# Performance work log

Hardware: AMD Instinct MI355X
Metric: run time of the kernel (lower is better)

Reference implementation:

```python
import jax, jax.numpy as jnp
import numpy as np

NUM_HEADS = 16
WINDOW = 256


def setup_inputs() -> dict:
    key = jax.random.key(0)
    ks = jax.random.split(key, 4)
    B, S, D = 1, 4096, 1024
    scale = 1.0 / np.sqrt(D)  # keep logits sane with random weights
    x = jax.random.normal(ks[0], (B, S, D), dtype=jnp.float32)
    Wq = jax.random.normal(ks[1], (D, D), dtype=jnp.float32) * scale
    Wk = jax.random.normal(ks[2], (D, D), dtype=jnp.float32) * scale
    Wv = jax.random.normal(ks[3], (D, D), dtype=jnp.float32) * scale
    bq = jnp.zeros((D,), dtype=jnp.float32)
    bk = jnp.zeros((D,), dtype=jnp.float32)
    bv = jnp.zeros((D,), dtype=jnp.float32)
    return {"x": x, "Wq": Wq, "bq": bq, "Wk": Wk, "bk": bk, "Wv": Wv, "bv": bv}


def reference(x, Wq, bq, Wk, bk, Wv, bv):
    B, S, D = x.shape
    H = NUM_HEADS
    depth = D // H

    def split_heads(t):
        return t.reshape(B, S, H, depth).transpose(0, 2, 1, 3)  # [B,H,S,depth]

    # torch nn.Linear: y = x @ W.T + b
    Q = split_heads(x @ Wq.T + bq)
    K = split_heads(x @ Wk.T + bk)
    V = split_heads(x @ Wv.T + bv)

    scores = jnp.einsum("bhqd,bhkd->bhqk", Q, K) / jnp.sqrt(jnp.float32(depth))
    idx = jnp.arange(S)
    band = jnp.abs(idx[None, :] - idx[:, None]) <= WINDOW  # [S,S] local window
    scores = jnp.where(band[None, None], scores, -jnp.inf)
    attn = jax.nn.softmax(scores, axis=-1)
    out = jnp.einsum("bhqk,bhkd->bhqd", attn, V)
    return out.transpose(0, 2, 1, 3).reshape(B, S, D)
```

## Files before the change

### kernel.cpp

```cpp
#include <hip/hip_runtime.h>
#include <hip/hip_bf16.h>

typedef __attribute__((ext_vector_type(4))) float f32x4;
typedef __attribute__((ext_vector_type(16))) float f32x16;
typedef __attribute__((ext_vector_type(8))) short s16x8;
typedef __attribute__((ext_vector_type(4))) float float4_t;
typedef __attribute__((ext_vector_type(2))) unsigned int u32x2;

union U8 { s16x8 v; unsigned u[4]; };

__device__ __forceinline__ ushort f2bf(float f) {
  union { float f; unsigned u; } v; v.f = f;
  unsigned r = v.u + 0x7fffu + ((v.u >> 16) & 1u);
  return (ushort)(r >> 16);
}

__device__ __forceinline__ void async_copy16(ushort* lds, const ushort* g) {
  __builtin_amdgcn_global_load_lds(
      (const __attribute__((address_space(1))) unsigned int*)g,
      (__attribute__((address_space(3))) unsigned int*)lds, 16, 0, 0);
}

__device__ __forceinline__ unsigned lds_addr(const void* p) {
  return (unsigned)(unsigned long long)(__attribute__((address_space(3))) const void*)p;
}

#define TRRD(dst, addr, off_lit) \
  asm volatile("ds_read_b64_tr_b16 %0, %1 offset:" #off_lit : "=v"(dst) : "v"(addr))

__global__ __launch_bounds__(256) void convert_kernel(
    const float* __restrict__ x, const float* __restrict__ Wq,
    const float* __restrict__ Wk, const float* __restrict__ Wv,
    ushort* __restrict__ xs, ushort* __restrict__ ws) {
  int b = blockIdx.x;
  if (b < 2048) {
    int c = b * 256 + threadIdx.x;
    int kc = c & 127;
    int m = c >> 7;
    const float4_t* s = (const float4_t*)&x[(size_t)m * 1024 + kc * 8];
    float4_t a0 = s[0], a1 = s[1];
    s16x8 v;
    v[0] = (short)f2bf(a0[0]); v[1] = (short)f2bf(a0[1]);
    v[2] = (short)f2bf(a0[2]); v[3] = (short)f2bf(a0[3]);
    v[4] = (short)f2bf(a1[0]); v[5] = (short)f2bf(a1[1]);
    v[6] = (short)f2bf(a1[2]); v[7] = (short)f2bf(a1[3]);
    int tm = m >> 7, tk = kc >> 3, r = m & 127, c8 = kc & 7;
    *(s16x8*)&xs[((size_t)(tm * 16 + tk) * 128 + r) * 64 + ((c8 ^ (r & 7)) * 8)] = v;
  } else {
    int c = (b - 2048) * 256 + threadIdx.x;
    int kc = c & 127;
    int n = c >> 7;
    int p = n >> 10, nW = n & 1023;
    const float* __restrict__ W = (p == 0) ? Wq : (p == 1) ? Wk : Wv;
    const float4_t* s = (const float4_t*)&W[(size_t)nW * 1024 + kc * 8];
    float4_t a0 = s[0], a1 = s[1];
    s16x8 v;
    v[0] = (short)f2bf(a0[0]); v[1] = (short)f2bf(a0[1]);
    v[2] = (short)f2bf(a0[2]); v[3] = (short)f2bf(a0[3]);
    v[4] = (short)f2bf(a1[0]); v[5] = (short)f2bf(a1[1]);
    v[6] = (short)f2bf(a1[2]); v[7] = (short)f2bf(a1[3]);
    unsigned tn3 = (unsigned)n / 192u;
    unsigned r = (unsigned)n - tn3 * 192u;
    int tk = kc >> 3, c8 = kc & 7;
    *(s16x8*)&ws[((size_t)(tn3 * 16 + tk) * 192 + r) * 64 + ((c8 ^ (r & 7)) * 8)] = v;
  }
}

__global__ __launch_bounds__(256, 2) void qkv_gemm_kernel(
    const ushort* __restrict__ xs, const ushort* __restrict__ wsb,
    const float* __restrict__ bq, const float* __restrict__ bk,
    const float* __restrict__ bv, ushort* __restrict__ qkv) {
  __shared__ ushort lA[2][8192];
  __shared__ ushort lB[2][12288];
  const int t = threadIdx.x;
  const int lane = t & 63, w = t >> 6;
  const int wm = w >> 1, wn = w & 1;
  const int l15 = lane & 15, l4 = lane >> 4;
  const int phys = blockIdx.x;
  const int swz = (phys & 7) * 64 + (phys >> 3);
  const int xcd = swz >> 6, jj = swz & 63;
  const int bm = (xcd >> 1) * 8 + (jj >> 3);
  const int bn = (xcd & 1) * 8 + (jj & 7);

  const ushort* Apan = xs + (size_t)bm * 16 * 8192;
  const ushort* Bpan = wsb + (size_t)bn * 16 * 12288;

  f32x4 acc[4][6];
#pragma unroll
  for (int i = 0; i < 4; i++)
#pragma unroll
    for (int j = 0; j < 6; j++) acc[i][j] = (f32x4)0.f;

#define STAGE_A(buf, kt)                                                        \
  do {                                                                          \
    const ushort* s0 = Apan + (size_t)(kt) * 8192;                              \
    _Pragma("unroll") for (int i_ = 0; i_ < 4; i_++)                            \
      async_copy16(&lA[buf][(t + i_ * 256) * 8], s0 + (t + i_ * 256) * 8);      \
  } while (0)
#define STAGE_B(buf, kt)                                                        \
  do {                                                                          \
    const ushort* s2 = Bpan + (size_t)(kt) * 12288;                             \
    _Pragma("unroll") for (int i_ = 0; i_ < 6; i_++)                            \
      async_copy16(&lB[buf][(t + i_ * 256) * 8], s2 + (t + i_ * 256) * 8);      \
  } while (0)

  STAGE_A(0, 0);
  STAGE_B(0, 0);
  asm volatile("s_waitcnt vmcnt(0)");
  __builtin_amdgcn_s_barrier();

  for (int kt = 0; kt < 16; ++kt) {
    const int cur = kt & 1;
    s16x8 af[4], bfr[6];
#pragma unroll
    for (int mi = 0; mi < 4; mi++) {
      int ra = wm * 64 + mi * 16 + l15;
      int g = l4 ^ (ra & 7);
      af[mi] = *(const s16x8*)&lA[cur][ra * 64 + g * 8];
    }
#pragma unroll
    for (int ni = 0; ni < 6; ni++) {
      int rb = wn * 96 + ni * 16 + l15;
      int g = l4 ^ (rb & 7);
      bfr[ni] = *(const s16x8*)&lB[cur][rb * 64 + g * 8];
    }
    if (kt + 1 < 16) STAGE_A(cur ^ 1, kt + 1);
    asm volatile("s_waitcnt lgkmcnt(0)");
    __builtin_amdgcn_sched_barrier(0);
    __builtin_amdgcn_s_setprio(1);
#pragma unroll
    for (int mi = 0; mi < 4; mi++)
#pragma unroll
      for (int ni = 0; ni < 6; ni++)
        acc[mi][ni] = __builtin_amdgcn_mfma_f32_16x16x32_bf16(af[mi], bfr[ni], acc[mi][ni], 0, 0, 0);
    __builtin_amdgcn_s_setprio(0);
#pragma unroll
    for (int mi = 0; mi < 4; mi++) {
      int ra = wm * 64 + mi * 16 + l15;
      int g = (4 + l4) ^ (ra & 7);
      af[mi] = *(const s16x8*)&lA[cur][ra * 64 + g * 8];
    }
#pragma unroll
    for (int ni = 0; ni < 6; ni++) {
      int rb = wn * 96 + ni * 16 + l15;
      int g = (4 + l4) ^ (rb & 7);
      bfr[ni] = *(const s16x8*)&lB[cur][rb * 64 + g * 8];
    }
    if (kt + 1 < 16) STAGE_B(cur ^ 1, kt + 1);
    asm volatile("s_waitcnt lgkmcnt(0)");
    __builtin_amdgcn_sched_barrier(0);
    __builtin_amdgcn_s_setprio(1);
#pragma unroll
    for (int mi = 0; mi < 4; mi++)
#pragma unroll
      for (int ni = 0; ni < 6; ni++)
        acc[mi][ni] = __builtin_amdgcn_mfma_f32_16x16x32_bf16(af[mi], bfr[ni], acc[mi][ni], 0, 0, 0);
    __builtin_amdgcn_s_setprio(0);
    asm volatile("s_waitcnt vmcnt(0)");
    __builtin_amdgcn_s_barrier();
  }
#undef STAGE_A
#undef STAGE_B

#pragma unroll
  for (int ni = 0; ni < 6; ni++) {
    int col = bn * 192 + wn * 96 + ni * 16 + l15;
    int p = col >> 10;
    const float* bias = (p == 0) ? bq : (p == 1) ? bk : bv;
    float b = bias[col & 1023];
    float qscale = (p == 0) ? 0.125f * 1.44269504f : 1.0f;
    int h = (col >> 6) & 15, dd = col & 63;
    size_t base = ((size_t)(p * 16 + h) * 4096) * 64 + dd;
#pragma unroll
    for (int mi = 0; mi < 4; mi++) {
#pragma unroll
      for (int r = 0; r < 4; r++) {
        int s = bm * 128 + wm * 64 + mi * 16 + l4 * 4 + r;
        float v = (acc[mi][ni][r] + b) * qscale;
        qkv[base + (size_t)s * 64] = f2bf(v);
      }
    }
  }
}

__global__ __launch_bounds__(256) void attn_local_kernel(
    const ushort* __restrict__ qkv, float* __restrict__ out) {
  __shared__ ushort lds[2][2][4096];
  const int bid = blockIdx.x;
  const int wid = (bid & 7) * 64 + (bid >> 3);
  const int hd = wid >> 5;
  const int q0 = (wid & 31) << 7;
  const int t = threadIdx.x;
  const int lane = t & 63, w = t >> 6;
  const int l15 = lane & 15, l31 = lane & 31;
  const int b4 = (lane >> 4) & 1, hf = lane >> 5;
  const int qw = q0 + w * 32;
  const int myq = qw + l31;

  const ushort* __restrict__ Q = qkv;
  const ushort* __restrict__ K = qkv + (size_t)16 * 4096 * 64;
  const ushort* __restrict__ V = K + (size_t)16 * 4096 * 64;

  s16x8 qf[4];
  {
    const ushort* qp = &Q[((size_t)hd * 4096 + myq) * 64];
#pragma unroll
    for (int kc = 0; kc < 4; kc++) qf[kc] = *(const s16x8*)&qp[16 * kc + 8 * hf];
  }

  U8 ones;
  {
    unsigned w1 = (l31 == 0) ? 0x3F803F80u : 0u;
    ones.u[0] = w1; ones.u[1] = w1; ones.u[2] = w1; ones.u[3] = w1;
  }

  f32x16 oa0 = (f32x16)0.f, oa1 = (f32x16)0.f, oden = (f32x16)0.f;

  const unsigned vtr0 = lds_addr(&lds[0][1][0]) +
      (unsigned)(hf * 1024 + (l15 >> 2) * 128 + b4 * 32 + (l15 & 3) * 8);

  int kstart = q0 - 256; if (kstart < 0) kstart = 0;
  int kend = q0 + 384; if (kend > 4096) kend = 4096;

#define STAGE_KV(buf, kb)                                                      \
  do {                                                                         \
    const ushort* Kg = &K[((size_t)hd * 4096 + (kb)) * 64];                    \
    const ushort* Vg = &V[((size_t)hd * 4096 + (kb)) * 64];                    \
    _Pragma("unroll") for (int i = 0; i < 2; i++) {                            \
      int off = i * 2048 + t * 8;                                              \
      int row = off >> 6;                                                      \
      int c8s = (off >> 3) & 7;                                                \
      async_copy16(&lds[buf][0][off], &Kg[row * 64 + ((c8s ^ (row & 7)) * 8)]);\
      async_copy16(&lds[buf][1][off], &Vg[off]);                               \
    }                                                                          \
  } while (0)

  STAGE_KV(0, kstart);
  asm volatile("s_waitcnt vmcnt(0)");
  __builtin_amdgcn_s_barrier();

  for (int kb = kstart; kb < kend; kb += 64) {
    const int cur = ((kb - kstart) >> 6) & 1;
    if (kb + 64 < kend) {
      if (cur) STAGE_KV(0, kb + 64); else STAGE_KV(1, kb + 64);
    }
    bool active = (kb + 63 >= qw - 256) && (kb <= qw + 31 + 256);
    if (active) {
      const ushort* lK = &lds[cur][0][0];
      f32x16 st0 = (f32x16)0.f, st1 = (f32x16)0.f;
      __builtin_amdgcn_s_setprio(1);
#pragma unroll
      for (int kc = 0; kc < 4; kc++) {
        int c8 = 2 * kc + hf;
        int r0 = l31;
        s16x8 kf0 = *(const s16x8*)&lK[r0 * 64 + ((c8 ^ (r0 & 7)) * 8)];
        st0 = __builtin_amdgcn_mfma_f32_32x32x16_bf16(kf0, qf[kc], st0, 0, 0, 0);
        int r1 = 32 + l31;
        s16x8 kf1 = *(const s16x8*)&lK[r1 * 64 + ((c8 ^ (r1 & 7)) * 8)];
        st1 = __builtin_amdgcn_mfma_f32_32x32x16_bf16(kf1, qf[kc], st1, 0, 0, 0);
      }
      __builtin_amdgcn_s_setprio(0);
      const bool interior = (kb >= qw - 225) && (kb <= qw + 193);
      if (!interior) {
        int base0 = myq - kb - 4 * hf + 256;
#pragma unroll
        for (int r = 0; r < 16; r++) {
          int ko = (r & 3) + 8 * (r >> 2);
          if (!((unsigned)(base0 - ko) <= 512u)) st0[r] = -3e38f;
          if (!((unsigned)(base0 - 32 - ko) <= 512u)) st1[r] = -3e38f;
        }
      }
      const unsigned vtr = vtr0 + (unsigned)cur * 16384u;
      u32x2 v0, v1, v2, v3, v4, v5, v6, v7, v8, v9, v10, v11, v12, v13, v14, v15;
      TRRD(v0, vtr, 0);     TRRD(v1, vtr, 512);  TRRD(v2, vtr, 64);    TRRD(v3, vtr, 576);
      TRRD(v4, vtr, 2048);  TRRD(v5, vtr, 2560); TRRD(v6, vtr, 2112);  TRRD(v7, vtr, 2624);
      TRRD(v8, vtr, 4096);  TRRD(v9, vtr, 4608); TRRD(v10, vtr, 4160); TRRD(v11, vtr, 4672);
      TRRD(v12, vtr, 6144); TRRD(v13, vtr, 6656); TRRD(v14, vtr, 6208); TRRD(v15, vtr, 6720);
      U8 pa0, pa1, pa2, pa3;
#define PACK(STV, RB, OUT)                                                     \
  do {                                                                         \
    float e0 = __builtin_amdgcn_exp2f(STV[RB + 0]);                            \
    float e1 = __builtin_amdgcn_exp2f(STV[RB + 1]);                            \
    float e2 = __builtin_amdgcn_exp2f(STV[RB + 2]);                            \
    float e3 = __builtin_amdgcn_exp2f(STV[RB + 3]);                            \
    float e4 = __builtin_amdgcn_exp2f(STV[RB + 4]);                            \
    float e5 = __builtin_amdgcn_exp2f(STV[RB + 5]);                            \
    float e6 = __builtin_amdgcn_exp2f(STV[RB + 6]);                            \
    float e7 = __builtin_amdgcn_exp2f(STV[RB + 7]);                            \
    unsigned a0, a1, b0, b1;                                                   \
    asm("v_cvt_pk_bf16_f32 %0, %1, %2" : "=v"(a0) : "v"(e0), "v"(e1));         \
    asm("v_cvt_pk_bf16_f32 %0, %1, %2" : "=v"(a1) : "v"(e2), "v"(e3));         \
    asm("v_cvt_pk_bf16_f32 %0, %1, %2" : "=v"(b0) : "v"(e4), "v"(e5));         \
    asm("v_cvt_pk_bf16_f32 %0, %1, %2" : "=v"(b1) : "v"(e6), "v"(e7));         \
    asm volatile("v_permlane32_swap_b32 %0, %1" : "+v"(a0), "+v"(b0));         \
    asm volatile("v_permlane32_swap_b32 %0, %1" : "+v"(a1), "+v"(b1));         \
    OUT.u[0] = a0; OUT.u[1] = a1; OUT.u[2] = b0; OUT.u[3] = b1;                \
  } while (0)
      PACK(st0, 0, pa0); PACK(st0, 8, pa1); PACK(st1, 0, pa2); PACK(st1, 8, pa3);
#undef PACK
#define MFMA3(PA, VA0, VA1, VB0, VB1)                                          \
  do {                                                                         \
    U8 f0, f1;                                                                 \
    f0.u[0] = VA0[0]; f0.u[1] = VA0[1]; f0.u[2] = VA1[0]; f0.u[3] = VA1[1];    \
    f1.u[0] = VB0[0]; f1.u[1] = VB0[1]; f1.u[2] = VB1[0]; f1.u[3] = VB1[1];    \
    __builtin_amdgcn_s_setprio(1);                                             \
    oa0 = __builtin_amdgcn_mfma_f32_32x32x16_bf16(PA.v, f0.v, oa0, 0, 0, 0);   \
    oa1 = __builtin_amdgcn_mfma_f32_32x32x16_bf16(PA.v, f1.v, oa1, 0, 0, 0);   \
    oden = __builtin_amdgcn_mfma_f32_32x32x16_bf16(PA.v, ones.v, oden, 0, 0, 0);\
    __builtin_amdgcn_s_setprio(0);                                             \
  } while (0)
      asm volatile("s_waitcnt lgkmcnt(12)");
      __builtin_amdgcn_sched_barrier(0);
      MFMA3(pa0, v0, v1, v2, v3);
      asm volatile("s_waitcnt lgkmcnt(8)");
      __builtin_amdgcn_sched_barrier(0);
      MFMA3(pa1, v4, v5, v6, v7);
      asm volatile("s_waitcnt lgkmcnt(4)");
      __builtin_amdgcn_sched_barrier(0);
      MFMA3(pa2, v8, v9, v10, v11);
      asm volatile("s_waitcnt lgkmcnt(0)");
      __builtin_amdgcn_sched_barrier(0);
      MFMA3(pa3, v12, v13, v14, v15);
#undef MFMA3
    }
    asm volatile("s_waitcnt vmcnt(0)");
    __builtin_amdgcn_s_barrier();
  }
#undef STAGE_KV
#pragma unroll
  for (int r = 0; r < 16; r++) {
    float den = __shfl(oden[r], lane & 32);
    float linv = 1.0f / den;
    int s = qw + (r & 3) + 8 * (r >> 2) + 4 * hf;
    out[(size_t)s * 1024 + hd * 64 + l31] = oa0[r] * linv;
    out[(size_t)s * 1024 + hd * 64 + 32 + l31] = oa1[r] * linv;
  }
}

extern "C" void kernel_launch(void* const* d_in, const int* in_sizes, int n_in,
                              void* d_out, int out_size, void* d_ws, size_t ws_size,
                              hipStream_t stream) {
  const float* x  = (const float*)d_in[0];
  const float* Wq = (const float*)d_in[1];
  const float* bq = (const float*)d_in[2];
  const float* Wk = (const float*)d_in[3];
  const float* bk = (const float*)d_in[4];
  const float* Wv = (const float*)d_in[5];
  const float* bv = (const float*)d_in[6];

  ushort* qkv = (ushort*)d_ws;
  ushort* xs  = (ushort*)((char*)d_ws + (size_t)25165824);
  ushort* wsb = xs + (size_t)4096 * 1024;
  float* out = (float*)d_out;

  convert_kernel<<<3584, 256, 0, stream>>>(x, Wq, Wk, Wv, xs, wsb);
  qkv_gemm_kernel<<<512, 256, 0, stream>>>(xs, wsb, bq, bk, bv, qkv);
  attn_local_kernel<<<512, 256, 0, stream>>>(qkv, out);
}
```

Baseline: 60.05 us.

## Split attention key range across two wave groups per block with LDS reduction

Doubles the attention block to 512 threads, forming two groups of four waves. Each group processes alternate 64-key tiles for the same 128 queries, with its own double-buffered LDS staging. The unnormalized outputs and denominators are then summed through LDS before the final normalization and store. This is meant to halve the serial key loop per wave and raise occupancy. The cost is double the LDS, an extra reduction pass with a block-wide sync, and more register pressure under launch bounds of 512.

Result: faster. 58.34 us, median of 3 (-2.8%).

```diff
diff --git a/kernel.cpp b/kernel.cpp
--- a/kernel.cpp
+++ b/kernel.cpp
@@ -183,18 +183,20 @@
   }
 }
 
-__global__ __launch_bounds__(256) void attn_local_kernel(
+__global__ __launch_bounds__(512) void attn_local_kernel(
     const ushort* __restrict__ qkv, float* __restrict__ out) {
-  __shared__ ushort lds[2][2][4096];
+  __shared__ ushort lds[2][2][2][4096];
   const int bid = blockIdx.x;
   const int wid = (bid & 7) * 64 + (bid >> 3);
   const int hd = wid >> 5;
   const int q0 = (wid & 31) << 7;
   const int t = threadIdx.x;
   const int lane = t & 63, w = t >> 6;
+  const int g = w >> 2, wl = w & 3;
+  const int tl = t & 255;
   const int l15 = lane & 15, l31 = lane & 31;
   const int b4 = (lane >> 4) & 1, hf = lane >> 5;
-  const int qw = q0 + w * 32;
+  const int qw = q0 + wl * 32;
   const int myq = qw + l31;
 
   const ushort* __restrict__ Q = qkv;
@@ -216,37 +218,37 @@
 
   f32x16 oa0 = (f32x16)0.f, oa1 = (f32x16)0.f, oden = (f32x16)0.f;
 
-  const unsigned vtr0 = lds_addr(&lds[0][1][0]) +
+  const unsigned vtr0 = lds_addr(&lds[g][0][1][0]) +
       (unsigned)(hf * 1024 + (l15 >> 2) * 128 + b4 * 32 + (l15 & 3) * 8);
 
   int kstart = q0 - 256; if (kstart < 0) kstart = 0;
   int kend = q0 + 384; if (kend > 4096) kend = 4096;
-
-#define STAGE_KV(buf, kb)                                                      \
+  const int R = (kend - kstart) >> 7;
+
+#define STAGE_KV(d, kb)                                                        \
   do {                                                                         \
     const ushort* Kg = &K[((size_t)hd * 4096 + (kb)) * 64];                    \
     const ushort* Vg = &V[((size_t)hd * 4096 + (kb)) * 64];                    \
-    _Pragma("unroll") for (int i = 0; i < 2; i++) {                            \
-      int off = i * 2048 + t * 8;                                              \
+    _Pragma("unroll") for (int i_ = 0; i_ < 2; i_++) {                         \
+      int off = i_ * 2048 + tl * 8;                                            \
       int row = off >> 6;                                                      \
       int c8s = (off >> 3) & 7;                                                \
-      async_copy16(&lds[buf][0][off], &Kg[row * 64 + ((c8s ^ (row & 7)) * 8)]);\
-      async_copy16(&lds[buf][1][off], &Vg[off]);                               \
+      async_copy16(&lds[g][d][0][off], &Kg[row * 64 + ((c8s ^ (row & 7)) * 8)]);\
+      async_copy16(&lds[g][d][1][off], &Vg[off]);                              \
     }                                                                          \
   } while (0)
 
-  STAGE_KV(0, kstart);
+  STAGE_KV(0, kstart + g * 64);
   asm volatile("s_waitcnt vmcnt(0)");
   __builtin_amdgcn_s_barrier();
 
-  for (int kb = kstart; kb < kend; kb += 64) {
-    const int cur = ((kb - kstart) >> 6) & 1;
-    if (kb + 64 < kend) {
-      if (cur) STAGE_KV(0, kb + 64); else STAGE_KV(1, kb + 64);
-    }
+  for (int j = 0; j < R; ++j) {
+    const int d = j & 1;
+    if (j + 1 < R) STAGE_KV(d ^ 1, kstart + (2 * (j + 1) + g) * 64);
+    const int kb = kstart + (2 * j + g) * 64;
     bool active = (kb + 63 >= qw - 256) && (kb <= qw + 31 + 256);
     if (active) {
-      const ushort* lK = &lds[cur][0][0];
+      const ushort* lK = &lds[g][d][0][0];
       f32x16 st0 = (f32x16)0.f, st1 = (f32x16)0.f;
       __builtin_amdgcn_s_setprio(1);
 #pragma unroll
@@ -270,7 +272,7 @@
           if (!((unsigned)(base0 - 32 - ko) <= 512u)) st1[r] = -3e38f;
         }
       }
-      const unsigned vtr = vtr0 + (unsigned)cur * 16384u;
+      const unsigned vtr = vtr0 + (unsigned)d * 16384u;
       u32x2 v0, v1, v2, v3, v4, v5, v6, v7, v8, v9, v10, v11, v12, v13, v14, v15;
       TRRD(v0, vtr, 0);     TRRD(v1, vtr, 512);  TRRD(v2, vtr, 64);    TRRD(v3, vtr, 576);
       TRRD(v4, vtr, 2048);  TRRD(v5, vtr, 2560); TRRD(v6, vtr, 2112);  TRRD(v7, vtr, 2624);
@@ -327,13 +329,34 @@
     __builtin_amdgcn_s_barrier();
   }
 #undef STAGE_KV
-#pragma unroll
-  for (int r = 0; r < 16; r++) {
-    float den = __shfl(oden[r], lane & 32);
-    float linv = 1.0f / den;
-    int s = qw + (r & 3) + 8 * (r >> 2) + 4 * hf;
-    out[(size_t)s * 1024 + hd * 64 + l31] = oa0[r] * linv;
-    out[(size_t)s * 1024 + hd * 64 + 32 + l31] = oa1[r] * linv;
+
+  float* red = (float*)&lds[0][0][0][0];
+  if (g == 1) {
+    int base = (wl * 64 + lane) * 49;
+#pragma unroll
+    for (int r = 0; r < 16; r++) {
+      red[base + r] = oa0[r];
+      red[base + 16 + r] = oa1[r];
+      red[base + 32 + r] = oden[r];
+    }
+  }
+  __syncthreads();
+  if (g == 0) {
+    int base = (wl * 64 + lane) * 49;
+#pragma unroll
+    for (int r = 0; r < 16; r++) {
+      oa0[r] += red[base + r];
+      oa1[r] += red[base + 16 + r];
+      oden[r] += red[base + 32 + r];
+    }
+#pragma unroll
+    for (int r = 0; r < 16; r++) {
+      float den = __shfl(oden[r], lane & 32);
+      float linv = 1.0f / den;
+      int s = qw + (r & 3) + 8 * (r >> 2) + 4 * hf;
+      out[(size_t)s * 1024 + hd * 64 + l31] = oa0[r] * linv;
+      out[(size_t)s * 1024 + hd * 64 + 32 + l31] = oa1[r] * linv;
+    }
   }
 }
 
@@ -355,5 +378,5 @@
 
   convert_kernel<<<3584, 256, 0, stream>>>(x, Wq, Wk, Wv, xs, wsb);
   qkv_gemm_kernel<<<512, 256, 0, stream>>>(xs, wsb, bq, bk, bv, qkv);
-  attn_local_kernel<<<512, 256, 0, stream>>>(qkv, out);
-}
+  attn_local_kernel<<<512, 512, 0, stream>>>(qkv, out);
+}
```
